# Kernel tuning notes

Measured on AMD Instinct MI355X. Metric: run time of the kernel, lower is better.

## Reference

```python
import jax, jax.numpy as jnp
import numpy as np

E, NH, NL, NP = 256, 8, 3, 4
HD = E // NH  # 32
SPATIAL = np.array([[100, 100], [50, 50], [25, 25]], dtype=np.int64)  # (H_l, W_l)


def setup_inputs() -> dict:
    key = jax.random.key(0)
    ks = jax.random.split(key, 12)
    Lv = int(SPATIAL.prod(1).sum())  # 13125
    B, Lq = 4, Lv
    query = jax.random.normal(ks[0], (B, Lq, E), jnp.float32)
    value = jax.random.normal(ks[1], (B, Lv, E), jnp.float32)
    reference_points = jax.random.uniform(ks[2], (B, Lq, NL, 2), dtype=jnp.float32)
    s = 1.0 / np.sqrt(E)
    Wv = jax.random.normal(ks[3], (E, E), jnp.float32) * s
    bv = jnp.zeros((E,), jnp.float32)
    Wo = jax.random.normal(ks[4], (E, E), jnp.float32) * s
    bo = jnp.zeros((E,), jnp.float32)
    # sampling_offsets: small random weight, grid-init bias (as in _reset_parameters)
    Woff = jax.random.normal(ks[5], (E, NH * NL * NP * 2), jnp.float32) * 0.01
    thetas = np.arange(NH, dtype=np.float32) * (2.0 * np.pi / NH)
    grid = np.stack([np.cos(thetas), np.sin(thetas)], -1)
    grid = grid / np.abs(grid).max(-1, keepdims=True)
    grid = np.tile(grid[:, None, None, :], (1, NL, NP, 1)) * np.arange(1, NP + 1, dtype=np.float32)[None, None, :, None]
    boff = jnp.asarray(grid.reshape(-1), jnp.float32)
    Watt = jax.random.normal(ks[6], (E, NH * NL * NP), jnp.float32) * 0.01
    batt = jnp.zeros((NH * NL * NP,), jnp.float32)
    return {
        "query": query, "reference_points": reference_points, "value": value,
        "value_spatial_shapes": jnp.asarray(SPATIAL),
        "Wv": Wv, "bv": bv, "Woff": Woff, "boff": boff,
        "Watt": Watt, "batt": batt, "Wo": Wo, "bo": bo,
    }


def _bilinear_sample(vl, x, y, Hl, Wl):
    """vl: (B, NH, Hl*Wl, HD); x, y: (B, Lq, NH, NP) pixel coords (align_corners=False).
    Returns (B, Lq, NH, NP, HD) with zero padding outside, matching F.grid_sample."""
    B, Lq = x.shape[0], x.shape[1]
    x0 = jnp.floor(x)
    y0 = jnp.floor(y)
    x0i = x0.astype(jnp.int32)
    y0i = y0.astype(jnp.int32)
    wx1 = x - x0
    wy1 = y - y0
    acc = jnp.zeros((B, Lq, NH, NP, HD), vl.dtype)
    for yi, wy in ((y0i, 1.0 - wy1), (y0i + 1, wy1)):
        for xi, wx in ((x0i, 1.0 - wx1), (x0i + 1, wx1)):
            valid = (xi >= 0) & (xi < Wl) & (yi >= 0) & (yi < Hl)
            idx = jnp.clip(yi, 0, Hl - 1) * Wl + jnp.clip(xi, 0, Wl - 1)  # (B,Lq,NH,NP)
            idxf = idx.transpose(0, 2, 1, 3).reshape(B, NH, Lq * NP)
            g = jnp.take_along_axis(vl, idxf[..., None], axis=2)  # (B,NH,Lq*NP,HD)
            g = g.reshape(B, NH, Lq, NP, HD).transpose(0, 2, 1, 3, 4)
            w = (wx * wy) * valid.astype(vl.dtype)
            acc = acc + g * w[..., None]
    return acc


def reference(query, reference_points, value, value_spatial_shapes,
              Wv, bv, Woff, boff, Watt, batt, Wo, bo):
    shapes = np.asarray(jax.device_get(value_spatial_shapes))  # static level metadata
    B, Lq, _ = query.shape
    v = value @ Wv + bv  # (B, Lv, E)
    v = v.reshape(B, -1, NH, HD)
    off = (query @ Woff + boff).reshape(B, Lq, NH, NL, NP, 2)
    aw = (query @ Watt + batt).reshape(B, Lq, NH, NL * NP)
    aw = jax.nn.softmax(aw, axis=-1).reshape(B, Lq, NH, NL, NP)
    # normalizer is (W_l, H_l)
    norm = jnp.asarray(np.stack([shapes[:, 1], shapes[:, 0]], -1), jnp.float32)  # (NL, 2)
    locs = reference_points[:, :, None, :, None, :] + off / norm[None, None, None, :, None, :]
    splits = np.cumsum(shapes.prod(1))[:-1].tolist()
    v_levels = jnp.split(v, splits, axis=1)
    out = jnp.zeros((B, Lq, NH, HD), v.dtype)
    for l in range(NL):
        Hl, Wl = int(shapes[l, 0]), int(shapes[l, 1])
        vl = v_levels[l].transpose(0, 2, 1, 3)  # (B, NH, Hl*Wl, HD)
        # grid_sample(align_corners=False): pixel = loc * size - 0.5
        x = locs[:, :, :, l, :, 0] * Wl - 0.5
        y = locs[:, :, :, l, :, 1] * Hl - 0.5
        samp = _bilinear_sample(vl, x, y, Hl, Wl)  # (B,Lq,NH,NP,HD)
        out = out + jnp.einsum('bqhpd,bqhp->bqhd', samp, aw[:, :, :, l, :])
    out = out.reshape(B, Lq, E)
    return out @ Wo + bo
```

## Files before the change

### kernel.cpp

```cpp
#include <hip/hip_runtime.h>
#include <hip/hip_bf16.h>
#include <hip/hip_fp16.h>

#define E    256
#define NH   8
#define NL   3
#define NP   4
#define HD   32
#define LQ   13125

typedef short bf16x8 __attribute__((ext_vector_type(8)));
typedef _Float16 f16x8 __attribute__((ext_vector_type(8)));
typedef float f32x4  __attribute__((ext_vector_type(4)));

__device__ __forceinline__ ushort f2bf(float x) {
  uint u = __float_as_uint(x);
  uint r = (u + 0x7fffu + ((u >> 16) & 1u)) >> 16;
  return (ushort)r;
}
__device__ __forceinline__ float bf2f(ushort u) {
  return __uint_as_float((uint)u << 16);
}
__device__ __forceinline__ ushort f2h(float x) {
  return __half_as_ushort(__float2half(x));
}
__device__ __forceinline__ __half2 u2h2(uint u) {
  union { uint u; __half2 h; } c; c.u = u; return c.h;
}
__device__ __forceinline__ uint h22u(__half2 h) {
  union { uint u; __half2 h; } c; c.h = h; return c.u;
}

__device__ __forceinline__ void gl_lds16(const ushort* g, ushort* l) {
  __builtin_amdgcn_global_load_lds(
      (const __attribute__((address_space(1))) void*)g,
      (__attribute__((address_space(3))) void*)l, 16, 0, 0);
}

__device__ __forceinline__ bf16x8 cvt8(const float* p) {
  const float4 a = *(const float4*)p;
  const float4 b = *(const float4*)(p + 4);
  bf16x8 r;
  r[0] = (short)f2bf(a.x); r[1] = (short)f2bf(a.y);
  r[2] = (short)f2bf(a.z); r[3] = (short)f2bf(a.w);
  r[4] = (short)f2bf(b.x); r[5] = (short)f2bf(b.y);
  r[6] = (short)f2bf(b.z); r[7] = (short)f2bf(b.w);
  return r;
}

__global__ __launch_bounds__(512) void gemm_wide_v(
    const float* __restrict__ A32, const ushort* __restrict__ B_,
    const float* __restrict__ bias, ushort* __restrict__ Cf16, int M) {
  __shared__ ushort As[4096];
  __shared__ ushort Bs[8192];
  const int tid = threadIdx.x;
  const int lane = tid & 63;
  const int wid = tid >> 6;
  const int wm = wid >> 2, wn = wid & 3;
  const int r0 = blockIdx.x * 128;
  const int l15 = lane & 15;
  const int lhi = lane >> 4;

  f32x4 acc[4][4] = {};

  for (int kk = 0; kk < 256; kk += 32) {
    {
      const int arow = min(r0 + (tid >> 2), M - 1);
      *(bf16x8*)&As[tid * 8] =
          cvt8(A32 + (size_t)arow * 256 + kk + (tid & 3) * 8);
    }
#pragma unroll
    for (int rr = 0; rr < 2; ++rr) {
      const int u = rr * 512 + tid;
      const int brow = u >> 2;
      gl_lds16(B_ + (size_t)brow * 256 + kk + (u & 3) * 8,
               Bs + rr * 4096 + wid * 512);
    }
    __syncthreads();

    bf16x8 af[4], bf[4];
#pragma unroll
    for (int mi = 0; mi < 4; ++mi)
      af[mi] = *(const bf16x8*)&As[(wm * 64 + mi * 16 + l15) * 32 + lhi * 8];
#pragma unroll
    for (int ni = 0; ni < 4; ++ni)
      bf[ni] = *(const bf16x8*)&Bs[(wn * 64 + ni * 16 + l15) * 32 + lhi * 8];
#pragma unroll
    for (int mi = 0; mi < 4; ++mi)
#pragma unroll
      for (int ni = 0; ni < 4; ++ni)
        acc[mi][ni] = __builtin_amdgcn_mfma_f32_16x16x32_bf16(
            af[mi], bf[ni], acc[mi][ni], 0, 0, 0);
    __syncthreads();
  }

#pragma unroll
  for (int ni = 0; ni < 4; ++ni) {
    const int col = wn * 64 + ni * 16 + l15;
    const float bb = bias[col];
    const int h = col >> 5, d = col & 31;
#pragma unroll
    for (int mi = 0; mi < 4; ++mi) {
      const int rowb = r0 + wm * 64 + mi * 16 + lhi * 4;
#pragma unroll
      for (int r = 0; r < 4; ++r) {
        const int row = rowb + r;
        if (row >= M) continue;
        const int bidx = row / LQ, pos = row - bidx * LQ;
        Cf16[((size_t)(bidx * NH + h) * LQ + pos) * HD + d] =
            f2h(acc[mi][ni][r] + bb);
      }
    }
  }
}

__global__ __launch_bounds__(512) void gemm_q_pack(
    const float* __restrict__ A32, const ushort* __restrict__ B_,
    const float* __restrict__ bias, const float* __restrict__ ref,
    uint* __restrict__ samp, int M) {
  __shared__ __align__(16) char ldsbuf[37 * 1024];
  ushort* As = (ushort*)ldsbuf;
  ushort* Bs = (ushort*)(ldsbuf + 8192);
  float* panel = (float*)ldsbuf;

  const int tid = threadIdx.x;
  const int lane = tid & 63;
  const int wid = tid >> 6;
  const int rg = wid >> 1;
  const int cg = wid & 1;
  const int r0 = blockIdx.x * 128;
  const int l15 = lane & 15;
  const int lhi = lane >> 4;

  f32x4 acc[2][9] = {};

  for (int kk = 0; kk < 256; kk += 32) {
    {
      const int arow = min(r0 + (tid >> 2), M - 1);
      *(bf16x8*)&As[tid * 8] =
          cvt8(A32 + (size_t)arow * 256 + kk + (tid & 3) * 8);
    }
#pragma unroll
    for (int rr = 0; rr < 3; ++rr) {
      const int u = rr * 512 + tid;
      if (u < 1152)
        gl_lds16(B_ + (size_t)(u >> 2) * 256 + kk + (u & 3) * 8,
                 Bs + (u >> 2) * 32 + (u & 3) * 8);
    }
    __syncthreads();

    bf16x8 af[2], bf[9];
#pragma unroll
    for (int mi = 0; mi < 2; ++mi)
      af[mi] = *(const bf16x8*)&As[(rg * 32 + mi * 16 + l15) * 32 + lhi * 8];
#pragma unroll
    for (int ni = 0; ni < 9; ++ni)
      bf[ni] = *(const bf16x8*)&Bs[(cg * 144 + ni * 16 + l15) * 32 + lhi * 8];
#pragma unroll
    for (int mi = 0; mi < 2; ++mi)
#pragma unroll
      for (int ni = 0; ni < 9; ++ni)
        acc[mi][ni] = __builtin_amdgcn_mfma_f32_16x16x32_bf16(
            af[mi], bf[ni], acc[mi][ni], 0, 0, 0);
    __syncthreads();
  }

  const float S_[3] = {100.f, 50.f, 25.f};
  const int Wl_[3] = {100, 50, 25};
#pragma unroll
  for (int c = 0; c < 4; ++c) {
    if (rg == c) {
#pragma unroll
      for (int mi = 0; mi < 2; ++mi)
#pragma unroll
        for (int ni = 0; ni < 9; ++ni) {
          const int col = cg * 144 + ni * 16 + l15;
          const float bb = bias[col];
          const int rl = mi * 16 + lhi * 4;
#pragma unroll
          for (int r = 0; r < 4; ++r)
            panel[(rl + r) * 289 + col] = acc[mi][ni][r] + bb;
        }
    }
    __syncthreads();
    if (tid < 256) {
      const int r = tid >> 3, h = tid & 7;
      const int g = r0 + c * 32 + r;
      if (g < M) {
        const float* rg_ = &panel[r * 289];
        float xy[24], lg[12];
#pragma unroll
        for (int j = 0; j < 24; ++j) xy[j] = rg_[h * 24 + j];
#pragma unroll
        for (int j = 0; j < 12; ++j) lg[j] = rg_[192 + h * 12 + j];
        float rx[3], ry[3];
#pragma unroll
        for (int l = 0; l < 3; ++l) {
          rx[l] = ref[(size_t)g * 6 + l * 2 + 0];
          ry[l] = ref[(size_t)g * 6 + l * 2 + 1];
        }
        float m = lg[0];
#pragma unroll
        for (int j = 1; j < 12; ++j) m = fmaxf(m, lg[j]);
        float e[12], s = 0.f;
#pragma unroll
        for (int j = 0; j < 12; ++j) { e[j] = __expf(lg[j] - m); s += e[j]; }
        const float inv = 1.f / s;

        uint out[36];
#pragma unroll
        for (int l = 0; l < 3; ++l) {
          const int Wl = Wl_[l];
#pragma unroll
          for (int p = 0; p < 4; ++p) {
            const int j = l * 4 + p;
            const float x = rx[l] * S_[l] + xy[l * 8 + p * 2 + 0] - 0.5f;
            const float y = ry[l] * S_[l] + xy[l * 8 + p * 2 + 1] - 0.5f;
            const float w = e[j] * inv;
            const float fx = floorf(x), fy = floorf(y);
            const int x0 = (int)fx, y0 = (int)fy;
            const float wx1 = x - fx, wy1 = y - fy;
            const float wx0 = 1.f - wx1, wy0 = 1.f - wy1;
            const int x0c = min(max(x0, 0), Wl - 1);
            const int x1c = min(max(x0 + 1, 0), Wl - 1);
            const int y0c = min(max(y0, 0), Wl - 1);
            const int y1c = min(max(y0 + 1, 0), Wl - 1);
            const float vx0 = (x0 >= 0 && x0 < Wl) ? wx0 : 0.f;
            const float vx1 = (x0 + 1 >= 0 && x0 + 1 < Wl) ? wx1 : 0.f;
            const float vy0 = (y0 >= 0 && y0 < Wl) ? wy0 : 0.f;
            const float vy1 = (y0 + 1 >= 0 && y0 + 1 < Wl) ? wy1 : 0.f;
            const int idx00 = y0c * Wl + x0c;
            const uint meta = (uint)(x1c - x0c) | ((uint)((y1c - y0c) * Wl) << 1);
            out[j * 3 + 0] = (uint)idx00 | (meta << 16);
            out[j * 3 + 1] = (uint)f2h(w * vy0 * vx0) | ((uint)f2h(w * vy0 * vx1) << 16);
            out[j * 3 + 2] = (uint)f2h(w * vy1 * vx0) | ((uint)f2h(w * vy1 * vx1) << 16);
          }
        }
        uint4* o4 = (uint4*)(samp + (size_t)g * 288 + h * 36);
#pragma unroll
        for (int i = 0; i < 9; ++i)
          o4[i] = make_uint4(out[i * 4 + 0], out[i * 4 + 1],
                             out[i * 4 + 2], out[i * 4 + 3]);
      }
    }
    __syncthreads();
  }
}

__global__ __launch_bounds__(512) void gemm_wide_o(
    const ushort* __restrict__ A16, const ushort* __restrict__ B_,
    const float* __restrict__ bias, float* __restrict__ C, int M) {
  __shared__ ushort As[4096];
  __shared__ ushort Bs[8192];
  const int tid = threadIdx.x;
  const int lane = tid & 63;
  const int wid = tid >> 6;
  const int wm = wid >> 2, wn = wid & 3;
  const int r0 = blockIdx.x * 128;
  const int l15 = lane & 15;
  const int lhi = lane >> 4;

  f32x4 acc[4][4] = {};

  for (int kk = 0; kk < 256; kk += 32) {
    {
      const int arow = min(r0 + wid * 16 + (lane >> 2), M - 1);
      gl_lds16(A16 + (size_t)arow * 256 + kk + (lane & 3) * 8,
               As + wid * 512);
    }
#pragma unroll
    for (int rr = 0; rr < 2; ++rr) {
      const int u = rr * 512 + tid;
      const int brow = u >> 2;
      gl_lds16(B_ + (size_t)brow * 256 + kk + (u & 3) * 8,
               Bs + rr * 4096 + wid * 512);
    }
    __syncthreads();

    f16x8 af[4], bf[4];
#pragma unroll
    for (int mi = 0; mi < 4; ++mi)
      af[mi] = *(const f16x8*)&As[(wm * 64 + mi * 16 + l15) * 32 + lhi * 8];
#pragma unroll
    for (int ni = 0; ni < 4; ++ni)
      bf[ni] = *(const f16x8*)&Bs[(wn * 64 + ni * 16 + l15) * 32 + lhi * 8];
#pragma unroll
    for (int mi = 0; mi < 4; ++mi)
#pragma unroll
      for (int ni = 0; ni < 4; ++ni)
        acc[mi][ni] = __builtin_amdgcn_mfma_f32_16x16x32_f16(
            af[mi], bf[ni], acc[mi][ni], 0, 0, 0);
    __syncthreads();
  }

#pragma unroll
  for (int ni = 0; ni < 4; ++ni) {
    const int col = wn * 64 + ni * 16 + l15;
    const float bb = bias[col];
#pragma unroll
    for (int mi = 0; mi < 4; ++mi) {
      const int rowb = r0 + wm * 64 + mi * 16 + lhi * 4;
#pragma unroll
      for (int r = 0; r < 4; ++r) {
        const int row = rowb + r;
        if (row < M) C[(size_t)row * 256 + col] = acc[mi][ni][r] + bb;
      }
    }
  }
}

__global__ __launch_bounds__(256) void convert_W(
    const float* __restrict__ Wv, const float* __restrict__ Woff,
    const float* __restrict__ Watt, const float* __restrict__ Wo,
    const float* __restrict__ boff, const float* __restrict__ batt,
    ushort* __restrict__ WvT, ushort* __restrict__ WcT,
    ushort* __restrict__ WoT, float* __restrict__ bias288) {
  const int t = blockIdx.x * 256 + threadIdx.x;
  if (t < 256 * 256) {
    const int n = t >> 8, k = t & 255;
    WvT[t] = f2bf(Wv[k * 256 + n]);
    WoT[t] = f2h(Wo[k * 256 + n]);
  }
  if (t < 288 * 256) {
    const int n = t >> 8, k = t & 255;
    const float w = (n < 192) ? Woff[k * 192 + n] : Watt[k * 96 + (n - 192)];
    WcT[t] = f2bf(w);
  }
  if (t < 288) bias288[t] = (t < 192) ? boff[t] : batt[t - 192];
}

__global__ __launch_bounds__(256) void deform_packed(
    const ushort* __restrict__ vbf, const uint* __restrict__ samp,
    ushort* __restrict__ mid, int nq) {
  const int tid = threadIdx.x;
  const int pair = blockIdx.x & 31;
  const int qc = blockIdx.x >> 5;
  const int q = qc * 32 + (tid >> 3);
  if (q >= nq) return;
  const int lane8 = tid & 7;
  const int xs = lane8 >> 2;
  const int cq = lane8 & 3;
  const int h = pair & 7;
  const int b = pair >> 3;
  const int g = b * nq + q;

  const uint4* sp = (const uint4*)(samp + (size_t)g * 288 + h * 36);
  const char* vb = (const char*)(vbf + ((size_t)pair * nq) * HD + cq * 8);

  uint4 s[9];
#pragma unroll
  for (int i = 0; i < 9; ++i) s[i] = sp[i];
  uint sd[36];
#pragma unroll
  for (int i = 0; i < 9; ++i) {
    sd[4 * i + 0] = s[i].x; sd[4 * i + 1] = s[i].y;
    sd[4 * i + 2] = s[i].z; sd[4 * i + 3] = s[i].w;
  }

  const int loff_[3] = {0, 10000, 12500};
  uint offA[12], offB[12], wp0[12], wp1[12];
#pragma unroll
  for (int j = 0; j < 12; ++j) {
    const uint d0 = sd[j * 3 + 0];
    const int idx00 = (int)(d0 & 0xffffu);
    const uint meta = d0 >> 16;
    const int dx = (int)(meta & 1u);
    const int dyW = (int)(meta >> 1);
    const uint d1 = sd[j * 3 + 1];
    const uint d2 = sd[j * 3 + 2];
    const uint w0_ = xs ? (d1 >> 16) : (d1 & 0xffffu);
    const uint w1_ = xs ? (d2 >> 16) : (d2 & 0xffffu);
    wp0[j] = w0_ | (w0_ << 16);
    wp1[j] = w1_ | (w1_ << 16);
    offA[j] = (uint)(loff_[j >> 2] + idx00 + (xs ? dx : 0)) * (HD * 2);
    offB[j] = offA[j] + (uint)dyW * (HD * 2);
  }

  __half2 A0 = __float2half2_rn(0.f), A1 = A0, A2 = A0, A3 = A0;

  uint4 qa0 = *(const uint4*)(vb + offA[0]);
  uint4 qa1 = *(const uint4*)(vb + offB[0]);
  uint4 qb0 = *(const uint4*)(vb + offA[1]);
  uint4 qb1 = *(const uint4*)(vb + offB[1]);
#pragma unroll
  for (int j = 0; j < 12; ++j) {
    uint4 c0, c1;
    if ((j & 1) == 0) { c0 = qa0; c1 = qa1; }
    else              { c0 = qb0; c1 = qb1; }
    if (j + 2 < 12) {
      if ((j & 1) == 0) {
        qa0 = *(const uint4*)(vb + offA[j + 2]);
        qa1 = *(const uint4*)(vb + offB[j + 2]);
      } else {
        qb0 = *(const uint4*)(vb + offA[j + 2]);
        qb1 = *(const uint4*)(vb + offB[j + 2]);
      }
    }
    const __half2 w0 = u2h2(wp0[j]);
    const __half2 w1 = u2h2(wp1[j]);
    A0 = __hfma2(w0, u2h2(c0.x), A0);
    A1 = __hfma2(w0, u2h2(c0.y), A1);
    A2 = __hfma2(w0, u2h2(c0.z), A2);
    A3 = __hfma2(w0, u2h2(c0.w), A3);
    A0 = __hfma2(w1, u2h2(c1.x), A0);
    A1 = __hfma2(w1, u2h2(c1.y), A1);
    A2 = __hfma2(w1, u2h2(c1.z), A2);
    A3 = __hfma2(w1, u2h2(c1.w), A3);
  }

  A0 = __hadd2(A0, u2h2(__shfl_xor(h22u(A0), 4)));
  A1 = __hadd2(A1, u2h2(__shfl_xor(h22u(A1), 4)));
  A2 = __hadd2(A2, u2h2(__shfl_xor(h22u(A2), 4)));
  A3 = __hadd2(A3, u2h2(__shfl_xor(h22u(A3), 4)));

  if (xs == 0) {
    uint4 o;
    o.x = h22u(A0); o.y = h22u(A1); o.z = h22u(A2); o.w = h22u(A3);
    *(uint4*)&mid[(size_t)g * E + h * HD + cq * 8] = o;
  }
}

extern "C" void kernel_launch(void* const* d_in, const int* in_sizes, int n_in,
                              void* d_out, int out_size, void* d_ws, size_t ws_size,
                              hipStream_t stream) {
  const float* query = (const float*)d_in[0];
  const float* refpt = (const float*)d_in[1];
  const float* value = (const float*)d_in[2];
  const float* Wv   = (const float*)d_in[4];
  const float* bv   = (const float*)d_in[5];
  const float* Woff = (const float*)d_in[6];
  const float* boff = (const float*)d_in[7];
  const float* Watt = (const float*)d_in[8];
  const float* batt = (const float*)d_in[9];
  const float* Wo   = (const float*)d_in[10];
  const float* bo   = (const float*)d_in[11];

  const int M = in_sizes[0] / E;
  const int nq = LQ;
  const int nb = M / nq;

  float* wsf   = (float*)d_ws;
  float* raw   = wsf;
  float* b288  = raw + (size_t)M * 288;
  ushort* mid  = (ushort*)(b288 + 288);
  ushort* vbf  = mid + (size_t)M * 256;
  ushort* wvT  = vbf + (size_t)M * 256;
  ushort* woT  = wvT + 65536;
  ushort* wcT  = woT + 65536;

  const int gridM = (M + 127) / 128;

  convert_W<<<288, 256, 0, stream>>>(Wv, Woff, Watt, Wo, boff, batt,
                                     wvT, wcT, woT, b288);
  gemm_wide_v<<<gridM, 512, 0, stream>>>(value, wvT, bv, vbf, M);
  gemm_q_pack<<<gridM, 512, 0, stream>>>(
      query, wcT, b288, refpt, (uint*)raw, M);
  const int qchunks = (nq + 31) / 32;
  deform_packed<<<qchunks * nb * NH, 256, 0, stream>>>(
      vbf, (const uint*)raw, mid, nq);
  gemm_wide_o<<<gridM, 512, 0, stream>>>(mid, woT, bo, (float*)d_out, M);
}
```

Baseline: 188.5 us.

## Split deformable sampling points across two thread groups per query

The deform kernel now gives each query 16 threads instead of 8, so each half handles 6 of the 12 sampling points. An extra xor-shuffle stage combines the two halves. The manual double-buffered prefetch is dropped in favour of a plain unrolled loop. This doubles the grid size and memory-level parallelism for the gather, at the cost of redundant sample-metadata loads and one more reduction step.

```diff
diff --git a/kernel.cpp b/kernel.cpp
--- a/kernel.cpp
+++ b/kernel.cpp
@@ -335,11 +335,12 @@
   const int tid = threadIdx.x;
   const int pair = blockIdx.x & 31;
   const int qc = blockIdx.x >> 5;
-  const int q = qc * 32 + (tid >> 3);
+  const int q = qc * 16 + (tid >> 4);
   if (q >= nq) return;
-  const int lane8 = tid & 7;
-  const int xs = lane8 >> 2;
-  const int cq = lane8 & 3;
+  const int lane16 = tid & 15;
+  const int sq = lane16 >> 3;
+  const int xs = (lane16 >> 2) & 1;
+  const int cq = lane16 & 3;
   const int h = pair & 7;
   const int b = pair >> 3;
   const int g = b * nq + q;
@@ -358,9 +359,10 @@
   }
 
   const int loff_[3] = {0, 10000, 12500};
-  uint offA[12], offB[12], wp0[12], wp1[12];
-#pragma unroll
-  for (int j = 0; j < 12; ++j) {
+  uint offA[6], offB[6], wp0[6], wp1[6];
+#pragma unroll
+  for (int t = 0; t < 6; ++t) {
+    const int j = 2 * t + sq;
     const uint d0 = sd[j * 3 + 0];
     const int idx00 = (int)(d0 & 0xffffu);
     const uint meta = d0 >> 16;
@@ -370,34 +372,19 @@
     const uint d2 = sd[j * 3 + 2];
     const uint w0_ = xs ? (d1 >> 16) : (d1 & 0xffffu);
     const uint w1_ = xs ? (d2 >> 16) : (d2 & 0xffffu);
-    wp0[j] = w0_ | (w0_ << 16);
-    wp1[j] = w1_ | (w1_ << 16);
-    offA[j] = (uint)(loff_[j >> 2] + idx00 + (xs ? dx : 0)) * (HD * 2);
-    offB[j] = offA[j] + (uint)dyW * (HD * 2);
+    wp0[t] = w0_ | (w0_ << 16);
+    wp1[t] = w1_ | (w1_ << 16);
+    offA[t] = (uint)(loff_[j >> 2] + idx00 + (xs ? dx : 0)) * (HD * 2);
+    offB[t] = offA[t] + (uint)dyW * (HD * 2);
   }
 
   __half2 A0 = __float2half2_rn(0.f), A1 = A0, A2 = A0, A3 = A0;
-
-  uint4 qa0 = *(const uint4*)(vb + offA[0]);
-  uint4 qa1 = *(const uint4*)(vb + offB[0]);
-  uint4 qb0 = *(const uint4*)(vb + offA[1]);
-  uint4 qb1 = *(const uint4*)(vb + offB[1]);
-#pragma unroll
-  for (int j = 0; j < 12; ++j) {
-    uint4 c0, c1;
-    if ((j & 1) == 0) { c0 = qa0; c1 = qa1; }
-    else              { c0 = qb0; c1 = qb1; }
-    if (j + 2 < 12) {
-      if ((j & 1) == 0) {
-        qa0 = *(const uint4*)(vb + offA[j + 2]);
-        qa1 = *(const uint4*)(vb + offB[j + 2]);
-      } else {
-        qb0 = *(const uint4*)(vb + offA[j + 2]);
-        qb1 = *(const uint4*)(vb + offB[j + 2]);
-      }
-    }
-    const __half2 w0 = u2h2(wp0[j]);
-    const __half2 w1 = u2h2(wp1[j]);
+#pragma unroll
+  for (int t = 0; t < 6; ++t) {
+    const uint4 c0 = *(const uint4*)(vb + offA[t]);
+    const uint4 c1 = *(const uint4*)(vb + offB[t]);
+    const __half2 w0 = u2h2(wp0[t]);
+    const __half2 w1 = u2h2(wp1[t]);
     A0 = __hfma2(w0, u2h2(c0.x), A0);
     A1 = __hfma2(w0, u2h2(c0.y), A1);
     A2 = __hfma2(w0, u2h2(c0.z), A2);
@@ -408,12 +395,16 @@
     A3 = __hfma2(w1, u2h2(c1.w), A3);
   }
 
+  A0 = __hadd2(A0, u2h2(__shfl_xor(h22u(A0), 8)));
+  A1 = __hadd2(A1, u2h2(__shfl_xor(h22u(A1), 8)));
+  A2 = __hadd2(A2, u2h2(__shfl_xor(h22u(A2), 8)));
+  A3 = __hadd2(A3, u2h2(__shfl_xor(h22u(A3), 8)));
   A0 = __hadd2(A0, u2h2(__shfl_xor(h22u(A0), 4)));
   A1 = __hadd2(A1, u2h2(__shfl_xor(h22u(A1), 4)));
   A2 = __hadd2(A2, u2h2(__shfl_xor(h22u(A2), 4)));
   A3 = __hadd2(A3, u2h2(__shfl_xor(h22u(A3), 4)));
 
-  if (xs == 0) {
+  if ((lane16 >> 2) == 0) {
     uint4 o;
     o.x = h22u(A0); o.y = h22u(A1); o.z = h22u(A2); o.w = h22u(A3);
     *(uint4*)&mid[(size_t)g * E + h * HD + cq * 8] = o;
@@ -455,8 +446,8 @@
   gemm_wide_v<<<gridM, 512, 0, stream>>>(value, wvT, bv, vbf, M);
   gemm_q_pack<<<gridM, 512, 0, stream>>>(
       query, wcT, b288, refpt, (uint*)raw, M);
-  const int qchunks = (nq + 31) / 32;
-  deform_packed<<<qchunks * nb * NH, 256, 0, stream>>>(
+  const int qchunks = (nq + 15) / 16;
+  deform_packed<<<qchunks * 32, 256, 0, stream>>>(
       vbf, (const uint*)raw, mid, nq);
   gemm_wide_o<<<gridM, 512, 0, stream>>>(mid, woT, bo, (float*)d_out, M);
 }
```

After: 477.1 us. +153.1%, slower.
